# Kernel optimization log

Measured on AMD Instinct MI355X. Metric: run time of the kernel, lower is better.

Reference implementation:

```python
import jax, jax.numpy as jnp
import numpy as np


def _sepconv1x1(x, dw, pw, b):
    # SeparableConv2D with kernel=1: depthwise 1x1 = per-channel scale, then pointwise matmul
    return jnp.einsum('nhwc,cd->nhwd', x * dw, pw) + b


def setup_inputs() -> dict:
    key = jax.random.key(0)
    ks = jax.random.split(key, 12)
    N, H, W, C_in, C_red = 4, 64, 64, 256, 64
    s = 0.05  # small init so softmax logits are well-conditioned
    return {
        'feature_maps': jax.random.normal(ks[0], (N, H, W, C_in), jnp.float32),
        'global_channel_output': jax.random.normal(ks[1], (N, H, W, C_in), jnp.float32),
        'dw_q': jax.random.normal(ks[2], (C_in,), jnp.float32) * s,
        'pw_q': jax.random.normal(ks[3], (C_in, C_red), jnp.float32) * s,
        'b_q': jnp.zeros((C_red,), jnp.float32),
        'dw_k': jax.random.normal(ks[4], (C_in,), jnp.float32) * s,
        'pw_k': jax.random.normal(ks[5], (C_in, C_red), jnp.float32) * s,
        'b_k': jnp.zeros((C_red,), jnp.float32),
        'dw_v': jax.random.normal(ks[6], (C_in,), jnp.float32) * s,
        'pw_v': jax.random.normal(ks[7], (C_in, C_red), jnp.float32) * s,
        'b_v': jnp.zeros((C_red,), jnp.float32),
        'dw_a': jax.random.normal(ks[8], (C_red,), jnp.float32) * s,
        'pw_a': jax.random.normal(ks[9], (C_red, C_in), jnp.float32) * s,
        'b_a': jnp.zeros((C_in,), jnp.float32),
    }


def reference(feature_maps, global_channel_output,
              dw_q, pw_q, b_q, dw_k, pw_k, b_k, dw_v, pw_v, b_v,
              dw_a, pw_a, b_a):
    N, H, W, _ = feature_maps.shape
    q = _sepconv1x1(feature_maps, dw_q, pw_q, b_q)  # [N,H,W,Cr]
    k = _sepconv1x1(feature_maps, dw_k, pw_k, b_k)
    v = _sepconv1x1(feature_maps, dw_v, pw_v, b_v)
    Cr = q.shape[-1]
    q = q.reshape(N, H * W, Cr)
    k = k.reshape(N, H * W, Cr)
    v = v.reshape(N, H * W, Cr)
    # tf.matmul(key, query, transpose_b=True): scores[i,j] = key_i . query_j
    scores = jnp.einsum('nic,njc->nij', k, q)  # [N,HW,HW]
    scores = jax.nn.softmax(scores, axis=-1)
    # tf.matmul(value, scores, transpose_a=True) -> [N,Cr,HW]
    att = jnp.einsum('nic,nij->ncj', v, scores)
    # faithful raw reshape (as in the original TF code) from [N,Cr,HW] to [N,H,W,Cr]
    att = att.reshape(N, H, W, Cr)
    att = _sepconv1x1(att, dw_a, pw_a, b_a)  # [N,H,W,C_in]
    return global_channel_output * att + global_channel_output
```

## Files before the change

### kernel.cpp

```cpp
#include <hip/hip_runtime.h>
#include <hip/hip_bf16.h>

typedef __attribute__((ext_vector_type(8))) __bf16 bf16x8;
typedef __attribute__((ext_vector_type(2))) __bf16 bf16x2;
typedef __attribute__((ext_vector_type(4))) float floatx4;
typedef __attribute__((ext_vector_type(4))) unsigned short us4;
typedef __attribute__((ext_vector_type(8))) unsigned short us8;
typedef __attribute__((ext_vector_type(4))) short s16x4;
typedef __attribute__((ext_vector_type(2))) unsigned int uint2v;
typedef __attribute__((ext_vector_type(4))) unsigned int uint4v;

#define MFMA16(A, B, C) __builtin_amdgcn_mfma_f32_16x16x32_bf16((A), (B), (C), 0, 0, 0)
#define MFMA1K(A, B, C) __builtin_amdgcn_mfma_f32_16x16x16bf16_1k((A), (B), (C), 0, 0, 0)

#define LOG2E 1.44269504088896340736f

#if __has_builtin(__builtin_amdgcn_exp2f)
#define EXP2F(x) __builtin_amdgcn_exp2f(x)
#else
#define EXP2F(x) exp2f(x)
#endif

static __device__ __forceinline__ unsigned short f2bfbits(float f) {
    __hip_bfloat16 h = __float2bfloat16(f);
    union { __hip_bfloat16 h; unsigned short u; } cv;
    cv.h = h;
    return cv.u;
}
static __device__ __forceinline__ unsigned int rne32(float f) {
    unsigned int u = __builtin_bit_cast(unsigned int, f);
    return u + 0x7fffu + ((u >> 16) & 1u);
}
static __device__ __forceinline__ unsigned short rne16(float f) {
    return (unsigned short)(rne32(f) >> 16);
}

#if __has_builtin(__builtin_amdgcn_cvt_pk_bf16_f32)
static __device__ __forceinline__ s16x4 pack4(float e0, float e1, float e2, float e3) {
    bf16x2 lo = __builtin_amdgcn_cvt_pk_bf16_f32(e0, e1);
    bf16x2 hi = __builtin_amdgcn_cvt_pk_bf16_f32(e2, e3);
    uint2v u = {__builtin_bit_cast(unsigned int, lo), __builtin_bit_cast(unsigned int, hi)};
    return __builtin_bit_cast(s16x4, u);
}
static __device__ __forceinline__ bf16x8 cvt8(floatx4 a, floatx4 b) {
    bf16x2 p0 = __builtin_amdgcn_cvt_pk_bf16_f32(a[0], a[1]);
    bf16x2 p1 = __builtin_amdgcn_cvt_pk_bf16_f32(a[2], a[3]);
    bf16x2 p2 = __builtin_amdgcn_cvt_pk_bf16_f32(b[0], b[1]);
    bf16x2 p3 = __builtin_amdgcn_cvt_pk_bf16_f32(b[2], b[3]);
    uint4v u = {__builtin_bit_cast(unsigned int, p0), __builtin_bit_cast(unsigned int, p1),
                __builtin_bit_cast(unsigned int, p2), __builtin_bit_cast(unsigned int, p3)};
    return __builtin_bit_cast(bf16x8, u);
}
#else
static __device__ __forceinline__ s16x4 pack4(float e0, float e1, float e2, float e3) {
    unsigned int pa = __builtin_amdgcn_perm(rne32(e1), rne32(e0), 0x07060302u);
    unsigned int pb = __builtin_amdgcn_perm(rne32(e3), rne32(e2), 0x07060302u);
    uint2v u = {pa, pb};
    return __builtin_bit_cast(s16x4, u);
}
static __device__ __forceinline__ bf16x8 cvt8(floatx4 a, floatx4 b) {
    us8 u;
#pragma unroll
    for (int i = 0; i < 4; i++) { u[i] = rne16(a[i]); u[4 + i] = rne16(b[i]); }
    return __builtin_bit_cast(bf16x8, u);
}
#endif

static __device__ __forceinline__ bf16x8 load_bf8(const __hip_bfloat16* p) {
    return *reinterpret_cast<const bf16x8*>(p);
}
static __device__ __forceinline__ float bf2f(unsigned short u) {
    unsigned int w = ((unsigned int)u) << 16;
    return __builtin_bit_cast(float, w);
}

static __device__ __forceinline__ void gld16(const void* g, void* l) {
    __builtin_amdgcn_global_load_lds(
        (const __attribute__((address_space(1))) unsigned int*)g,
        (__attribute__((address_space(3))) unsigned int*)l, 16, 0, 0);
}


__global__ __launch_bounds__(256) void proj_qkv(
    const float* __restrict__ x,
    const float* __restrict__ dwq, const float* __restrict__ pwq,
    const float* __restrict__ dwk, const float* __restrict__ pwk,
    const float* __restrict__ dwv, const float* __restrict__ pwv,
    const float* __restrict__ bqp, const float* __restrict__ bkp,
    const float* __restrict__ bvp,
    __hip_bfloat16* __restrict__ qf, __hip_bfloat16* __restrict__ kf,
    __hip_bfloat16* __restrict__ vf)
{
    __shared__ __hip_bfloat16 wle[16384];
    int b = blockIdx.x;
    int p = b >> 8;
    int tg = b & 255;
    int tid = threadIdx.x;

    const float* dw = (p == 0) ? dwq : ((p == 1) ? dwk : dwv);
    const float* pw = (p == 0) ? pwq : ((p == 1) ? pwk : pwv);
    float scale = (p == 1) ? LOG2E : 1.0f;

    {
        float dwc = dw[tid];
#pragma unroll
        for (int k = 0; k < 64; k++) {
            int idx = (k * 256 + tid) ^ ((k & 7) << 3);
            wle[idx] = __float2bfloat16(dwc * pw[tid * 64 + k] * scale);
        }
    }
    __syncthreads();

    int wv = tid >> 6;
    int wid = tg * 4 + wv;
    int lane = tid & 63;
    int l15 = lane & 15, quad = lane >> 4;

    floatx4 acc[4];
#pragma unroll
    for (int t = 0; t < 4; t++) acc[t] = (floatx4){0.f, 0.f, 0.f, 0.f};

    const float* xrow = x + (wid * 16 + l15) * 256 + quad * 8;
#pragma unroll
    for (int ks = 0; ks < 8; ks++) {
        floatx4 xa = *reinterpret_cast<const floatx4*>(xrow + ks * 32);
        floatx4 xb = *reinterpret_cast<const floatx4*>(xrow + ks * 32 + 4);
        bf16x8 a = cvt8(xa, xb);
#pragma unroll
        for (int t = 0; t < 4; t++) {
            int j0 = ((t * 16 + l15) * 256 + ks * 32 + quad * 8) ^ ((l15 & 7) << 3);
            bf16x8 bfr = *reinterpret_cast<const bf16x8*>(&wle[j0]);
            acc[t] = MFMA16(a, bfr, acc[t]);
        }
    }
    if (p < 2) {
        __hip_bfloat16* dst = (p == 0) ? qf : kf;
        const float* bias = (p == 0) ? bqp : bkp;
        float bscale = (p == 1) ? LOG2E : 1.0f;
#pragma unroll
        for (int t = 0; t < 4; t++) {
            float bsv = bias[t * 16 + l15] * bscale;
            int off0 = wid * 1024 + (t >> 1) * 512 +
                       (((((t & 1) << 1) | (l15 >> 3)) * 16 + quad * 4) * 8) + (l15 & 7);
#pragma unroll
            for (int r = 0; r < 4; r++)
                dst[off0 + r * 8] = __float2bfloat16(acc[t][r] + bsv);
        }
    } else {
#pragma unroll
        for (int t = 0; t < 4; t++) {
            float bsv = bvp[t * 16 + l15];
            us4 pk;
#pragma unroll
            for (int r = 0; r < 4; r++) pk[r] = f2bfbits(acc[t][r] + bsv);
            *reinterpret_cast<us4*>(vf + (wid * 4 + t) * 256 + lane * 4) = pk;
        }
    }
}

#define P1STEP(B0, B1, B2, B3) do {                                        \
    floatx4 z = (floatx4){0.f, 0.f, 0.f, 0.f};                             \
    floatx4 sA0 = MFMA16(a1, (B1), MFMA16(a0, (B0), z));                   \
    floatx4 sA1 = MFMA16(a1, (B3), MFMA16(a0, (B2), z));                   \
    floatx4 sB0 = MFMA16(a3, (B1), MFMA16(a2, (B0), z));                   \
    floatx4 sB1 = MFMA16(a3, (B3), MFMA16(a2, (B2), z));                   \
    _Pragma("unroll")                                                      \
    for (int r = 0; r < 4; r++) {                                          \
        lsA[r] += EXP2F(sA0[r]) + EXP2F(sA1[r]);                           \
        lsB[r] += EXP2F(sB0[r]) + EXP2F(sB1[r]);                           \
    }                                                                      \
} while (0)

__global__ __launch_bounds__(512) void pass1_rl(
    const __hip_bfloat16* __restrict__ qf, const __hip_bfloat16* __restrict__ kf,
    const __hip_bfloat16* __restrict__ vf, __hip_bfloat16* __restrict__ vfs)
{
    int itg0 = blockIdx.x * 2;
    int n = itg0 >> 8;
    int jw = threadIdx.x >> 6;
    int lane = threadIdx.x & 63;
    int l15 = lane & 15, quad = lane >> 4;

    const __hip_bfloat16* kp = kf + itg0 * 1024 + lane * 8;
    bf16x8 a0 = load_bf8(kp);
    bf16x8 a1 = load_bf8(kp + 512);
    bf16x8 a2 = load_bf8(kp + 1024);
    bf16x8 a3 = load_bf8(kp + 1536);

    floatx4 lsA = (floatx4){0.f, 0.f, 0.f, 0.f};
    floatx4 lsB = (floatx4){0.f, 0.f, 0.f, 0.f};
    const __hip_bfloat16* qp0 = qf + (n * 256 + jw * 32) * 1024 + lane * 8;

    bf16x8 s0b0 = load_bf8(qp0);
    bf16x8 s0b1 = load_bf8(qp0 + 512);
    bf16x8 s0b2 = load_bf8(qp0 + 1024);
    bf16x8 s0b3 = load_bf8(qp0 + 1536);
    bf16x8 s1b0 = load_bf8(qp0 + 2048);
    bf16x8 s1b1 = load_bf8(qp0 + 2560);
    bf16x8 s1b2 = load_bf8(qp0 + 3072);
    bf16x8 s1b3 = load_bf8(qp0 + 3584);

    for (int it = 0; it < 16; it += 2) {
        bf16x8 n0 = load_bf8(qp0 + 4096);
        bf16x8 n1 = load_bf8(qp0 + 4608);
        bf16x8 n2 = load_bf8(qp0 + 5120);
        bf16x8 n3 = load_bf8(qp0 + 5632);
        P1STEP(s0b0, s0b1, s0b2, s0b3);
        s0b0 = n0; s0b1 = n1; s0b2 = n2; s0b3 = n3;
        bf16x8 m0 = load_bf8(qp0 + 6144);
        bf16x8 m1 = load_bf8(qp0 + 6656);
        bf16x8 m2 = load_bf8(qp0 + 7168);
        bf16x8 m3 = load_bf8(qp0 + 7680);
        P1STEP(s1b0, s1b1, s1b2, s1b3);
        s1b0 = m0; s1b1 = m1; s1b2 = m2; s1b3 = m3;
        qp0 += 4096;
    }
#pragma unroll
    for (int m = 1; m < 16; m <<= 1) {
#pragma unroll
        for (int r = 0; r < 4; r++) {
            lsA[r] += __shfl_xor(lsA[r], m, 64);
            lsB[r] += __shfl_xor(lsB[r], m, 64);
        }
    }
    __shared__ float red[8][32];
    __shared__ float rls[32];
    if (l15 == 0) {
#pragma unroll
        for (int r = 0; r < 4; r++) {
            red[jw][quad * 4 + r] = lsA[r];
            red[jw][16 + quad * 4 + r] = lsB[r];
        }
    }
    __syncthreads();
    if (threadIdx.x < 32) {
        float tot = 0.f;
#pragma unroll
        for (int w = 0; w < 8; w++) tot += red[w][threadIdx.x];
        rls[threadIdx.x] = 1.0f / tot;
    }
    __syncthreads();
    int m0 = threadIdx.x * 4;
    int toff = m0 >> 10;
    int mm = m0 & 1023;
    int t = mm >> 8;
    int l = (mm >> 2) & 63;
    int rb = toff * 16 + (l >> 4) * 4;
    us4 vv = *reinterpret_cast<const us4*>(
        reinterpret_cast<const unsigned short*>(vf) + itg0 * 1024 + m0);
    us4 ov;
#pragma unroll
    for (int r = 0; r < 4; r++) ov[r] = rne16(bf2f(vv[r]) * rls[rb + r]);
    int oidx = (t >> 1) * 512 + l * 8 + (t & 1) * 4;
    *reinterpret_cast<us4*>(
        reinterpret_cast<unsigned short*>(vfs) + (itg0 + toff) * 1024 + oidx) = ov;
}

#define P2STEP(KA, KB, VA, VB) do {                                            \
    floatx4 z = (floatx4){0.f, 0.f, 0.f, 0.f};                                 \
    floatx4 s0 = MFMA16((KB), bq0b, MFMA16((KA), bq0a, z));                    \
    floatx4 s1 = MFMA16((KB), bq1b, MFMA16((KA), bq1a, z));                    \
    floatx4 s2 = MFMA16((KB), bq2b, MFMA16((KA), bq2a, z));                    \
    floatx4 s3 = MFMA16((KB), bq3b, MFMA16((KA), bq3a, z));                    \
    s16x4 p0 = pack4(EXP2F(s0[0]), EXP2F(s0[1]), EXP2F(s0[2]), EXP2F(s0[3])); \
    s16x4 p1 = pack4(EXP2F(s1[0]), EXP2F(s1[1]), EXP2F(s1[2]), EXP2F(s1[3])); \
    s16x4 p2 = pack4(EXP2F(s2[0]), EXP2F(s2[1]), EXP2F(s2[2]), EXP2F(s2[3])); \
    s16x4 p3 = pack4(EXP2F(s3[0]), EXP2F(s3[1]), EXP2F(s3[2]), EXP2F(s3[3])); \
    s16x4 bv0 = __builtin_bit_cast(s16x4, __builtin_shufflevector((VA), (VA), 0, 1, 2, 3)); \
    s16x4 bv1 = __builtin_bit_cast(s16x4, __builtin_shufflevector((VA), (VA), 4, 5, 6, 7)); \
    s16x4 bv2 = __builtin_bit_cast(s16x4, __builtin_shufflevector((VB), (VB), 0, 1, 2, 3)); \
    s16x4 bv3 = __builtin_bit_cast(s16x4, __builtin_shufflevector((VB), (VB), 4, 5, 6, 7)); \
    acc0[0] = MFMA1K(p0, bv0, acc0[0]);                                        \
    acc1[0] = MFMA1K(p1, bv0, acc1[0]);                                        \
    acc2[0] = MFMA1K(p2, bv0, acc2[0]);                                        \
    acc3[0] = MFMA1K(p3, bv0, acc3[0]);                                        \
    acc0[1] = MFMA1K(p0, bv1, acc0[1]);                                        \
    acc1[1] = MFMA1K(p1, bv1, acc1[1]);                                        \
    acc2[1] = MFMA1K(p2, bv1, acc2[1]);                                        \
    acc3[1] = MFMA1K(p3, bv1, acc3[1]);                                        \
    acc0[2] = MFMA1K(p0, bv2, acc0[2]);                                        \
    acc1[2] = MFMA1K(p1, bv2, acc1[2]);                                        \
    acc2[2] = MFMA1K(p2, bv2, acc2[2]);                                        \
    acc3[2] = MFMA1K(p3, bv2, acc3[2]);                                        \
    acc0[3] = MFMA1K(p0, bv3, acc0[3]);                                        \
    acc1[3] = MFMA1K(p1, bv3, acc1[3]);                                        \
    acc2[3] = MFMA1K(p2, bv3, acc2[3]);                                        \
    acc3[3] = MFMA1K(p3, bv3, acc3[3]);                                        \
} while (0)

__global__ __launch_bounds__(512) void pass2_att(
    const __hip_bfloat16* __restrict__ qf, const __hip_bfloat16* __restrict__ kf,
    const __hip_bfloat16* __restrict__ vfs,
    unsigned short* __restrict__ attp)
{
    __shared__ char ldsbuf[2][8192];
    int b = blockIdx.x;
    int ih = b & 7;
    int jgrp = (b >> 3) & 7;
    int n = b >> 6;
    int tid = threadIdx.x;
    int w = tid >> 6;
    int lane = tid & 63;
    int l15 = lane & 15, quad = lane >> 4;
    int jt0 = jgrp * 32 + w * 4;

    const __hip_bfloat16* qp = qf + (n * 256 + jt0) * 1024 + lane * 8;
    bf16x8 bq0a = load_bf8(qp);
    bf16x8 bq0b = load_bf8(qp + 512);
    bf16x8 bq1a = load_bf8(qp + 1024);
    bf16x8 bq1b = load_bf8(qp + 1536);
    bf16x8 bq2a = load_bf8(qp + 2048);
    bf16x8 bq2b = load_bf8(qp + 2560);
    bf16x8 bq3a = load_bf8(qp + 3072);
    bf16x8 bq3b = load_bf8(qp + 3584);

    floatx4 acc0[4], acc1[4], acc2[4], acc3[4];
#pragma unroll
    for (int t = 0; t < 4; t++) {
        acc0[t] = (floatx4){0.f, 0.f, 0.f, 0.f};
        acc1[t] = (floatx4){0.f, 0.f, 0.f, 0.f};
        acc2[t] = (floatx4){0.f, 0.f, 0.f, 0.f};
        acc3[t] = (floatx4){0.f, 0.f, 0.f, 0.f};
    }

    int it0 = n * 256 + ih * 32;
    const char* gbase = (w < 4) ? (const char*)(kf + it0 * 1024)
                                : (const char*)(vfs + it0 * 1024);
    const char* gw = gbase + ((w >> 1) & 1) * 2048 + (w & 1) * 1024 + lane * 16;
    char* lw0 = &ldsbuf[0][w * 1024];
    char* lw1 = &ldsbuf[1][w * 1024];

    gld16(gw, lw0);
    __syncthreads();

    int cur = 0;
    for (int ph = 0; ph < 16; ph++) {
        if (ph < 15)
            gld16(gw + (ph + 1) * 4096, cur ? lw0 : lw1);
        const char* base = ldsbuf[cur];
#pragma unroll
        for (int t = 0; t < 2; t++) {
            bf16x8 a0 = *reinterpret_cast<const bf16x8*>(base + t * 2048 + lane * 16);
            bf16x8 a1 = *reinterpret_cast<const bf16x8*>(base + t * 2048 + 1024 + lane * 16);
            us8 v01 = *reinterpret_cast<const us8*>(base + 4096 + t * 2048 + lane * 16);
            us8 v23 = *reinterpret_cast<const us8*>(base + 4096 + t * 2048 + 1024 + lane * 16);
            P2STEP(a0, a1, v01, v23);
        }
        __syncthreads();
        cur ^= 1;
    }
    unsigned short* op0 = attp + ih * 1048576;
#pragma unroll
    for (int t = 0; t < 4; t++) {
        s16x4 k0 = pack4(acc0[t][0], acc0[t][1], acc0[t][2], acc0[t][3]);
        s16x4 k1 = pack4(acc1[t][0], acc1[t][1], acc1[t][2], acc1[t][3]);
        s16x4 k2 = pack4(acc2[t][0], acc2[t][1], acc2[t][2], acc2[t][3]);
        s16x4 k3 = pack4(acc3[t][0], acc3[t][1], acc3[t][2], acc3[t][3]);
        unsigned short* op = op0 + (n * 64 + t * 16 + l15) * 4096 + jt0 * 16 + quad * 4;
        *reinterpret_cast<s16x4*>(op) = k0;
        *reinterpret_cast<s16x4*>(op + 16) = k1;
        *reinterpret_cast<s16x4*>(op + 32) = k2;
        *reinterpret_cast<s16x4*>(op + 48) = k3;
    }
}

template<int NPART>
__global__ __launch_bounds__(256) void final_out(
    const unsigned short* __restrict__ attp, const float* __restrict__ gco,
    const float* __restrict__ dwa, const float* __restrict__ pwa,
    const float* __restrict__ ba, float* __restrict__ out)
{
    int b = blockIdx.x;
    int n = b >> 9;
    int hh = (b >> 3) & 63;
    int w0 = (b & 7) << 3;
    __shared__ float g[512];
    int tid = threadIdx.x;
    const unsigned short* ap = attp + (n * 64 + hh) * 4096 + w0 * 64;
    {
        int jj0 = tid * 2;
        float v0 = 0.f, v1 = 0.f;
#pragma unroll
        for (int ph = 0; ph < NPART; ph++) {
            unsigned int u = *reinterpret_cast<const unsigned int*>(ap + ph * 1048576 + jj0);
            v0 += bf2f((unsigned short)(u & 0xffffu));
            v1 += bf2f((unsigned short)(u >> 16));
        }
        g[jj0] = v0 * dwa[jj0 & 63];
        g[jj0 + 1] = v1 * dwa[(jj0 + 1) & 63];
    }
    __syncthreads();
    float acc[8];
#pragma unroll
    for (int w = 0; w < 8; w++) acc[w] = 0.f;
    for (int cc = 0; cc < 64; cc++) {
        float p = pwa[cc * 256 + tid];
#pragma unroll
        for (int w = 0; w < 8; w++) acc[w] += g[w * 64 + cc] * p;
    }
    float bb = ba[tid];
#pragma unroll
    for (int w = 0; w < 8; w++) {
        int pos = (n * 64 + hh) * 64 + w0 + w;
        float gv = gco[pos * 256 + tid];
        out[pos * 256 + tid] = gv * (acc[w] + bb) + gv;
    }
}

extern "C" void kernel_launch(void* const* d_in, const int* in_sizes, int n_in,
                              void* d_out, int out_size, void* d_ws, size_t ws_size,
                              hipStream_t stream) {
    const float* x   = (const float*)d_in[0];
    const float* gco = (const float*)d_in[1];
    const float* dwq = (const float*)d_in[2];
    const float* pwq = (const float*)d_in[3];
    const float* bq  = (const float*)d_in[4];
    const float* dwk = (const float*)d_in[5];
    const float* pwk = (const float*)d_in[6];
    const float* bk  = (const float*)d_in[7];
    const float* dwv = (const float*)d_in[8];
    const float* pwv = (const float*)d_in[9];
    const float* bv  = (const float*)d_in[10];
    const float* dwa = (const float*)d_in[11];
    const float* pwa = (const float*)d_in[12];
    const float* ba  = (const float*)d_in[13];
    float* out = (float*)d_out;

    char* ws = (char*)d_ws;
    __hip_bfloat16* qf  = (__hip_bfloat16*)(ws + 98304);
    __hip_bfloat16* kf  = (__hip_bfloat16*)(ws + 2195456);
    __hip_bfloat16* vf  = (__hip_bfloat16*)(ws + 4292608);
    __hip_bfloat16* vfs = (__hip_bfloat16*)(ws + 6389760);
    unsigned short* attp = (unsigned short*)(ws + 8486912);

    proj_qkv<<<768, 256, 0, stream>>>(x, dwq, pwq, dwk, pwk, dwv, pwv,
                                      bq, bk, bv, qf, kf, vf);
    pass1_rl<<<512, 512, 0, stream>>>(qf, kf, vf, vfs);
    pass2_att<<<256, 512, 0, stream>>>(qf, kf, vfs, attp);
    final_out<8><<<2048, 256, 0, stream>>>(attp, gco, dwa, pwa, ba, out);
}
```

Measured before the change: 165.7 us.

## Apply softmax row normalization inside pass2 instead of prescaling V in pass1

Pass1 now computes only the reciprocal row sums and writes them to a small float buffer. It no longer reads V and writes a rescaled, re-laid-out copy. Each pass1 block now handles four key tiles with four waves, which doubles K-register reuse per Q load. Pass2 loads the reciprocals into LDS and multiplies the exponentials by them before packing to bf16, reading the original V layout directly. This removes a full V read/write round trip but adds a per-element multiply in pass2's inner loop, and it halves the pass1 grid and block size.

```diff
diff --git a/kernel.cpp b/kernel.cpp
--- a/kernel.cpp
+++ b/kernel.cpp
@@ -160,22 +160,28 @@
 
 #define P1STEP(B0, B1, B2, B3) do {                                        \
     floatx4 z = (floatx4){0.f, 0.f, 0.f, 0.f};                             \
-    floatx4 sA0 = MFMA16(a1, (B1), MFMA16(a0, (B0), z));                   \
-    floatx4 sA1 = MFMA16(a1, (B3), MFMA16(a0, (B2), z));                   \
-    floatx4 sB0 = MFMA16(a3, (B1), MFMA16(a2, (B0), z));                   \
-    floatx4 sB1 = MFMA16(a3, (B3), MFMA16(a2, (B2), z));                   \
+    floatx4 s0 = MFMA16(a1, (B1), MFMA16(a0, (B0), z));                    \
+    floatx4 s1 = MFMA16(a1, (B3), MFMA16(a0, (B2), z));                    \
+    floatx4 s2 = MFMA16(a3, (B1), MFMA16(a2, (B0), z));                    \
+    floatx4 s3 = MFMA16(a3, (B3), MFMA16(a2, (B2), z));                    \
+    floatx4 s4 = MFMA16(a5, (B1), MFMA16(a4, (B0), z));                    \
+    floatx4 s5 = MFMA16(a5, (B3), MFMA16(a4, (B2), z));                    \
+    floatx4 s6 = MFMA16(a7, (B1), MFMA16(a6, (B0), z));                    \
+    floatx4 s7 = MFMA16(a7, (B3), MFMA16(a6, (B2), z));                    \
     _Pragma("unroll")                                                      \
     for (int r = 0; r < 4; r++) {                                          \
-        lsA[r] += EXP2F(sA0[r]) + EXP2F(sA1[r]);                           \
-        lsB[r] += EXP2F(sB0[r]) + EXP2F(sB1[r]);                           \
+        ls0[r] += EXP2F(s0[r]) + EXP2F(s1[r]);                             \
+        ls1[r] += EXP2F(s2[r]) + EXP2F(s3[r]);                             \
+        ls2[r] += EXP2F(s4[r]) + EXP2F(s5[r]);                             \
+        ls3[r] += EXP2F(s6[r]) + EXP2F(s7[r]);                             \
     }                                                                      \
 } while (0)
 
-__global__ __launch_bounds__(512) void pass1_rl(
+__global__ __launch_bounds__(256) void pass1_rl(
     const __hip_bfloat16* __restrict__ qf, const __hip_bfloat16* __restrict__ kf,
-    const __hip_bfloat16* __restrict__ vf, __hip_bfloat16* __restrict__ vfs)
+    float* __restrict__ rl)
 {
-    int itg0 = blockIdx.x * 2;
+    int itg0 = blockIdx.x * 4;
     int n = itg0 >> 8;
     int jw = threadIdx.x >> 6;
     int lane = threadIdx.x & 63;
@@ -186,10 +192,16 @@
     bf16x8 a1 = load_bf8(kp + 512);
     bf16x8 a2 = load_bf8(kp + 1024);
     bf16x8 a3 = load_bf8(kp + 1536);
-
-    floatx4 lsA = (floatx4){0.f, 0.f, 0.f, 0.f};
-    floatx4 lsB = (floatx4){0.f, 0.f, 0.f, 0.f};
-    const __hip_bfloat16* qp0 = qf + (n * 256 + jw * 32) * 1024 + lane * 8;
+    bf16x8 a4 = load_bf8(kp + 2048);
+    bf16x8 a5 = load_bf8(kp + 2560);
+    bf16x8 a6 = load_bf8(kp + 3072);
+    bf16x8 a7 = load_bf8(kp + 3584);
+
+    floatx4 ls0 = (floatx4){0.f, 0.f, 0.f, 0.f};
+    floatx4 ls1 = (floatx4){0.f, 0.f, 0.f, 0.f};
+    floatx4 ls2 = (floatx4){0.f, 0.f, 0.f, 0.f};
+    floatx4 ls3 = (floatx4){0.f, 0.f, 0.f, 0.f};
+    const __hip_bfloat16* qp0 = qf + (n * 256 + jw * 64) * 1024 + lane * 8;
 
     bf16x8 s0b0 = load_bf8(qp0);
     bf16x8 s0b1 = load_bf8(qp0 + 512);
@@ -200,7 +212,7 @@
     bf16x8 s1b2 = load_bf8(qp0 + 3072);
     bf16x8 s1b3 = load_bf8(qp0 + 3584);
 
-    for (int it = 0; it < 16; it += 2) {
+    for (int it = 0; it < 32; it += 2) {
         bf16x8 n0 = load_bf8(qp0 + 4096);
         bf16x8 n1 = load_bf8(qp0 + 4608);
         bf16x8 n2 = load_bf8(qp0 + 5120);
@@ -219,81 +231,69 @@
     for (int m = 1; m < 16; m <<= 1) {
 #pragma unroll
         for (int r = 0; r < 4; r++) {
-            lsA[r] += __shfl_xor(lsA[r], m, 64);
-            lsB[r] += __shfl_xor(lsB[r], m, 64);
-        }
-    }
-    __shared__ float red[8][32];
-    __shared__ float rls[32];
+            ls0[r] += __shfl_xor(ls0[r], m, 64);
+            ls1[r] += __shfl_xor(ls1[r], m, 64);
+            ls2[r] += __shfl_xor(ls2[r], m, 64);
+            ls3[r] += __shfl_xor(ls3[r], m, 64);
+        }
+    }
+    __shared__ float red[4][64];
     if (l15 == 0) {
 #pragma unroll
         for (int r = 0; r < 4; r++) {
-            red[jw][quad * 4 + r] = lsA[r];
-            red[jw][16 + quad * 4 + r] = lsB[r];
+            red[jw][quad * 4 + r]      = ls0[r];
+            red[jw][16 + quad * 4 + r] = ls1[r];
+            red[jw][32 + quad * 4 + r] = ls2[r];
+            red[jw][48 + quad * 4 + r] = ls3[r];
         }
     }
     __syncthreads();
-    if (threadIdx.x < 32) {
-        float tot = 0.f;
-#pragma unroll
-        for (int w = 0; w < 8; w++) tot += red[w][threadIdx.x];
-        rls[threadIdx.x] = 1.0f / tot;
-    }
-    __syncthreads();
-    int m0 = threadIdx.x * 4;
-    int toff = m0 >> 10;
-    int mm = m0 & 1023;
-    int t = mm >> 8;
-    int l = (mm >> 2) & 63;
-    int rb = toff * 16 + (l >> 4) * 4;
-    us4 vv = *reinterpret_cast<const us4*>(
-        reinterpret_cast<const unsigned short*>(vf) + itg0 * 1024 + m0);
-    us4 ov;
-#pragma unroll
-    for (int r = 0; r < 4; r++) ov[r] = rne16(bf2f(vv[r]) * rls[rb + r]);
-    int oidx = (t >> 1) * 512 + l * 8 + (t & 1) * 4;
-    *reinterpret_cast<us4*>(
-        reinterpret_cast<unsigned short*>(vfs) + (itg0 + toff) * 1024 + oidx) = ov;
-}
-
-#define P2STEP(KA, KB, VA, VB) do {                                            \
+    if (threadIdx.x < 64) {
+        float tot = red[0][threadIdx.x] + red[1][threadIdx.x] +
+                    red[2][threadIdx.x] + red[3][threadIdx.x];
+        rl[itg0 * 16 + threadIdx.x] = 1.0f / tot;
+    }
+}
+
+#define P2STEP(KA, KB, V0, V1, V2, V3, RLQ) do {                               \
     floatx4 z = (floatx4){0.f, 0.f, 0.f, 0.f};                                 \
     floatx4 s0 = MFMA16((KB), bq0b, MFMA16((KA), bq0a, z));                    \
     floatx4 s1 = MFMA16((KB), bq1b, MFMA16((KA), bq1a, z));                    \
     floatx4 s2 = MFMA16((KB), bq2b, MFMA16((KA), bq2a, z));                    \
     floatx4 s3 = MFMA16((KB), bq3b, MFMA16((KA), bq3a, z));                    \
-    s16x4 p0 = pack4(EXP2F(s0[0]), EXP2F(s0[1]), EXP2F(s0[2]), EXP2F(s0[3])); \
-    s16x4 p1 = pack4(EXP2F(s1[0]), EXP2F(s1[1]), EXP2F(s1[2]), EXP2F(s1[3])); \
-    s16x4 p2 = pack4(EXP2F(s2[0]), EXP2F(s2[1]), EXP2F(s2[2]), EXP2F(s2[3])); \
-    s16x4 p3 = pack4(EXP2F(s3[0]), EXP2F(s3[1]), EXP2F(s3[2]), EXP2F(s3[3])); \
-    s16x4 bv0 = __builtin_bit_cast(s16x4, __builtin_shufflevector((VA), (VA), 0, 1, 2, 3)); \
-    s16x4 bv1 = __builtin_bit_cast(s16x4, __builtin_shufflevector((VA), (VA), 4, 5, 6, 7)); \
-    s16x4 bv2 = __builtin_bit_cast(s16x4, __builtin_shufflevector((VB), (VB), 0, 1, 2, 3)); \
-    s16x4 bv3 = __builtin_bit_cast(s16x4, __builtin_shufflevector((VB), (VB), 4, 5, 6, 7)); \
-    acc0[0] = MFMA1K(p0, bv0, acc0[0]);                                        \
-    acc1[0] = MFMA1K(p1, bv0, acc1[0]);                                        \
-    acc2[0] = MFMA1K(p2, bv0, acc2[0]);                                        \
-    acc3[0] = MFMA1K(p3, bv0, acc3[0]);                                        \
-    acc0[1] = MFMA1K(p0, bv1, acc0[1]);                                        \
-    acc1[1] = MFMA1K(p1, bv1, acc1[1]);                                        \
-    acc2[1] = MFMA1K(p2, bv1, acc2[1]);                                        \
-    acc3[1] = MFMA1K(p3, bv1, acc3[1]);                                        \
-    acc0[2] = MFMA1K(p0, bv2, acc0[2]);                                        \
-    acc1[2] = MFMA1K(p1, bv2, acc1[2]);                                        \
-    acc2[2] = MFMA1K(p2, bv2, acc2[2]);                                        \
-    acc3[2] = MFMA1K(p3, bv2, acc3[2]);                                        \
-    acc0[3] = MFMA1K(p0, bv3, acc0[3]);                                        \
-    acc1[3] = MFMA1K(p1, bv3, acc1[3]);                                        \
-    acc2[3] = MFMA1K(p2, bv3, acc2[3]);                                        \
-    acc3[3] = MFMA1K(p3, bv3, acc3[3]);                                        \
+    s16x4 p0 = pack4(EXP2F(s0[0]) * (RLQ)[0], EXP2F(s0[1]) * (RLQ)[1],         \
+                     EXP2F(s0[2]) * (RLQ)[2], EXP2F(s0[3]) * (RLQ)[3]);        \
+    s16x4 p1 = pack4(EXP2F(s1[0]) * (RLQ)[0], EXP2F(s1[1]) * (RLQ)[1],         \
+                     EXP2F(s1[2]) * (RLQ)[2], EXP2F(s1[3]) * (RLQ)[3]);        \
+    s16x4 p2 = pack4(EXP2F(s2[0]) * (RLQ)[0], EXP2F(s2[1]) * (RLQ)[1],         \
+                     EXP2F(s2[2]) * (RLQ)[2], EXP2F(s2[3]) * (RLQ)[3]);        \
+    s16x4 p3 = pack4(EXP2F(s3[0]) * (RLQ)[0], EXP2F(s3[1]) * (RLQ)[1],         \
+                     EXP2F(s3[2]) * (RLQ)[2], EXP2F(s3[3]) * (RLQ)[3]);        \
+    acc0[0] = MFMA1K(p0, (V0), acc0[0]);                                       \
+    acc1[0] = MFMA1K(p1, (V0), acc1[0]);                                       \
+    acc2[0] = MFMA1K(p2, (V0), acc2[0]);                                       \
+    acc3[0] = MFMA1K(p3, (V0), acc3[0]);                                       \
+    acc0[1] = MFMA1K(p0, (V1), acc0[1]);                                       \
+    acc1[1] = MFMA1K(p1, (V1), acc1[1]);                                       \
+    acc2[1] = MFMA1K(p2, (V1), acc2[1]);                                       \
+    acc3[1] = MFMA1K(p3, (V1), acc3[1]);                                       \
+    acc0[2] = MFMA1K(p0, (V2), acc0[2]);                                       \
+    acc1[2] = MFMA1K(p1, (V2), acc1[2]);                                       \
+    acc2[2] = MFMA1K(p2, (V2), acc2[2]);                                       \
+    acc3[2] = MFMA1K(p3, (V2), acc3[2]);                                       \
+    acc0[3] = MFMA1K(p0, (V3), acc0[3]);                                       \
+    acc1[3] = MFMA1K(p1, (V3), acc1[3]);                                       \
+    acc2[3] = MFMA1K(p2, (V3), acc2[3]);                                       \
+    acc3[3] = MFMA1K(p3, (V3), acc3[3]);                                       \
 } while (0)
 
 __global__ __launch_bounds__(512) void pass2_att(
     const __hip_bfloat16* __restrict__ qf, const __hip_bfloat16* __restrict__ kf,
-    const __hip_bfloat16* __restrict__ vfs,
+    const __hip_bfloat16* __restrict__ vf, const float* __restrict__ rl,
     unsigned short* __restrict__ attp)
 {
     __shared__ char ldsbuf[2][8192];
+    __shared__ float rl_lds[512];
     int b = blockIdx.x;
     int ih = b & 7;
     int jgrp = (b >> 3) & 7;
@@ -304,6 +304,12 @@
     int l15 = lane & 15, quad = lane >> 4;
     int jt0 = jgrp * 32 + w * 4;
 
+    int it0 = n * 256 + ih * 32;
+
+    if (tid < 128)
+        *reinterpret_cast<floatx4*>(&rl_lds[tid * 4]) =
+            *reinterpret_cast<const floatx4*>(&rl[it0 * 16 + tid * 4]);
+
     const __hip_bfloat16* qp = qf + (n * 256 + jt0) * 1024 + lane * 8;
     bf16x8 bq0a = load_bf8(qp);
     bf16x8 bq0b = load_bf8(qp + 512);
@@ -323,9 +329,8 @@
         acc3[t] = (floatx4){0.f, 0.f, 0.f, 0.f};
     }
 
-    int it0 = n * 256 + ih * 32;
     const char* gbase = (w < 4) ? (const char*)(kf + it0 * 1024)
-                                : (const char*)(vfs + it0 * 1024);
+                                : (const char*)(vf + it0 * 1024);
     const char* gw = gbase + ((w >> 1) & 1) * 2048 + (w & 1) * 1024 + lane * 16;
     char* lw0 = &ldsbuf[0][w * 1024];
     char* lw1 = &ldsbuf[1][w * 1024];
@@ -342,9 +347,14 @@
         for (int t = 0; t < 2; t++) {
             bf16x8 a0 = *reinterpret_cast<const bf16x8*>(base + t * 2048 + lane * 16);
             bf16x8 a1 = *reinterpret_cast<const bf16x8*>(base + t * 2048 + 1024 + lane * 16);
-            us8 v01 = *reinterpret_cast<const us8*>(base + 4096 + t * 2048 + lane * 16);
-            us8 v23 = *reinterpret_cast<const us8*>(base + 4096 + t * 2048 + 1024 + lane * 16);
-            P2STEP(a0, a1, v01, v23);
+            const char* vb = base + 4096 + t * 2048 + lane * 8;
+            s16x4 v0 = *reinterpret_cast<const s16x4*>(vb);
+            s16x4 v1 = *reinterpret_cast<const s16x4*>(vb + 512);
+            s16x4 v2 = *reinterpret_cast<const s16x4*>(vb + 1024);
+            s16x4 v3 = *reinterpret_cast<const s16x4*>(vb + 1536);
+            floatx4 rlq = *reinterpret_cast<const floatx4*>(
+                &rl_lds[(ph * 2 + t) * 16 + quad * 4]);
+            P2STEP(a0, a1, v0, v1, v2, v3, rlq);
         }
         __syncthreads();
         cur ^= 1;
@@ -430,12 +440,12 @@
     __hip_bfloat16* qf  = (__hip_bfloat16*)(ws + 98304);
     __hip_bfloat16* kf  = (__hip_bfloat16*)(ws + 2195456);
     __hip_bfloat16* vf  = (__hip_bfloat16*)(ws + 4292608);
-    __hip_bfloat16* vfs = (__hip_bfloat16*)(ws + 6389760);
+    float*          rlb = (float*)(ws + 6389760);
     unsigned short* attp = (unsigned short*)(ws + 8486912);
 
     proj_qkv<<<768, 256, 0, stream>>>(x, dwq, pwq, dwk, pwk, dwv, pwv,
                                       bq, bk, bv, qf, kf, vf);
-    pass1_rl<<<512, 512, 0, stream>>>(qf, kf, vf, vfs);
-    pass2_att<<<256, 512, 0, stream>>>(qf, kf, vfs, attp);
+    pass1_rl<<<256, 256, 0, stream>>>(qf, kf, rlb);
+    pass2_att<<<256, 512, 0, stream>>>(qf, kf, vf, rlb, attp);
     final_out<8><<<2048, 256, 0, stream>>>(attp, gco, dwa, pwa, ba, out);
 }
```

Measured after the change: 184.5 us. 11.4% more time.
